# Optimization experiments

Measured on AMD Instinct MI355X. Metric: run time of the kernel, lower is better.

Reference implementation:

```python
import jax, jax.numpy as jnp
import numpy as np
from jax import lax

B, T, C = 64, 1024, 256


def setup_inputs() -> dict:
    key = jax.random.key(0)
    k1, k2 = jax.random.split(key)
    sequences = jax.random.normal(k1, (B, T, C), dtype=jnp.float32)
    transitions = jax.random.normal(k2, (C, C), dtype=jnp.float32)
    return {"sequences": sequences, "transitions": transitions}


def _viterbi_decode(sequences, transitions):
    # sequences: [B, T, C] unary scores; transitions: [C_prev, C_cur]
    num_classes = sequences.shape[-1]
    emissions = jnp.swapaxes(sequences, 0, 1)  # [T, B, C]

    def fwd_step(alpha, emit):
        # alpha: [B, C_prev]; emit: [B, C_cur]
        m = alpha[:, :, None] + transitions[None, :, :]  # [B, C_prev, C_cur]
        bp = jnp.argmax(m, axis=1).astype(jnp.int32)     # [B, C_cur] backpointers
        new_alpha = jnp.max(m, axis=1) + emit            # [B, C_cur]
        return new_alpha, bp

    alpha, bps = lax.scan(fwd_step, emissions[0], emissions[1:])  # bps: [T-1, B, C]
    last_tag = jnp.argmax(alpha, axis=-1).astype(jnp.int32)       # [B]

    def back_step(tag, bp):
        # tag: [B] tag at t+1; bp: [B, C] backpointers computed at step t+1
        prev = jnp.take_along_axis(bp, tag[:, None], axis=1)[:, 0]
        return prev, prev

    _, tags = lax.scan(back_step, last_tag, bps, reverse=True)  # [T-1, B]
    full = jnp.concatenate([tags, last_tag[None, :]], axis=0)   # [T, B]
    return jnp.swapaxes(full, 0, 1)  # [B, T]


def reference(sequences, transitions):
    # Inference path of CRF.call: viterbi decode + one-hot over num_classes.
    tags = _viterbi_decode(sequences, transitions)
    return jax.nn.one_hot(tags, sequences.shape[-1], dtype=sequences.dtype)
```

## Files before the change

### kernel.cpp

```cpp
#include <hip/hip_runtime.h>

#define Bn 64
#define Tn 1024
#define Cn 256

#define FWD_SYNC()                                  \
  do {                                              \
    __builtin_amdgcn_sched_barrier(0);              \
    __builtin_amdgcn_s_waitcnt(0xC07F);             \
    __builtin_amdgcn_s_barrier();                   \
    __builtin_amdgcn_sched_barrier(0);              \
  } while (0)

template<int CTRL>
__device__ __forceinline__ float dpp_mov_f(float x) {
  return __int_as_float(__builtin_amdgcn_update_dpp(0, __float_as_int(x), CTRL, 0xF, 0xF, true));
}
template<int CTRL>
__device__ __forceinline__ void max_stage(float& v) {
  const float pv = __int_as_float(__builtin_amdgcn_update_dpp(
      (int)0xFF800000, __float_as_int(v), CTRL, 0xF, 0xF, false));
  v = fmaxf(v, pv);
}

__device__ __forceinline__ int argmax64_fast(float v, int i) {
  float mv = v;
  max_stage<0x111>(mv);
  max_stage<0x112>(mv);
  max_stage<0x114>(mv);
  max_stage<0x118>(mv);
  max_stage<0x142>(mv);
  max_stage<0x143>(mv);
  const float smax = __int_as_float(__builtin_amdgcn_readlane(__float_as_int(mv), 63));
  const unsigned long long m = __ballot(v == smax);
  const int ln = __ffsll((unsigned long long)m) - 1;
  return __builtin_amdgcn_readlane(i, ln);
}

__device__ __forceinline__ int apad(int m) { return (m >> 2) * 20 + (m & 3) * 4; }

__global__ __launch_bounds__(1024) void crf_fwd_kernel(
    float* __restrict__ seq, const float* __restrict__ trans,
    float* __restrict__ transT, int useT) {
  __shared__ float lds[64 * 65];
  const int bi = blockIdx.x;
  const int tid = threadIdx.x;

  if (bi < Bn) {
    float* sb = seq + (size_t)bi * (Tn * Cn);
    const int l = tid & 63;
    const int w = tid >> 6;
    const int c = l & 15;
    const int g = l >> 4;
    const int ccb = w * 16 + g * 4;
    const int cpb = c * 16;
    float4 tr4[16];
#pragma unroll
    for (int k = 0; k < 16; ++k)
      tr4[k] = *(const float4*)(trans + (size_t)(cpb + k) * Cn + ccb);

    float* ab0 = lds;
    float* ab1 = lds + 320;
    if (tid < 64) *(float4*)(ab0 + apad(tid)) = ((const float4*)sb)[tid];
    const bool leader = (c == 0);
    const int woff = apad(w * 4 + g);
    float4 e4, pna;
    if (leader) e4 = *(const float4*)(sb + Cn + ccb);
    FWD_SYNC();

    for (int t = 1; t < Tn; ++t) {
      float4 pf;
      if (leader) {
        if (t > 1) *(float4*)(sb + (size_t)(t - 1) * Cn + ccb) = pna;
        const int tn = (t + 1 < Tn) ? (t + 1) : (Tn - 1);
        pf = *(const float4*)(sb + (size_t)tn * Cn + ccb);
      }
      const float* av = (t & 1) ? ab0 : ab1;
      float* aw = (t & 1) ? ab1 : ab0;
      const float* avc = av + c * 20;
      float m0 = -__builtin_inff(), m1 = m0, m2 = m0, m3 = m0;
#pragma unroll
      for (int j = 0; j < 4; ++j) {
        const float4 a = *(const float4*)(avc + j * 4);
        float4 t0 = tr4[4 * j + 0];
        m0 = fmaxf(m0, a.x + t0.x); m1 = fmaxf(m1, a.x + t0.y);
        m2 = fmaxf(m2, a.x + t0.z); m3 = fmaxf(m3, a.x + t0.w);
        float4 t1 = tr4[4 * j + 1];
        m0 = fmaxf(m0, a.y + t1.x); m1 = fmaxf(m1, a.y + t1.y);
        m2 = fmaxf(m2, a.y + t1.z); m3 = fmaxf(m3, a.y + t1.w);
        float4 t2 = tr4[4 * j + 2];
        m0 = fmaxf(m0, a.z + t2.x); m1 = fmaxf(m1, a.z + t2.y);
        m2 = fmaxf(m2, a.z + t2.z); m3 = fmaxf(m3, a.z + t2.w);
        float4 t3 = tr4[4 * j + 3];
        m0 = fmaxf(m0, a.w + t3.x); m1 = fmaxf(m1, a.w + t3.y);
        m2 = fmaxf(m2, a.w + t3.z); m3 = fmaxf(m3, a.w + t3.w);
      }
      m0 = fmaxf(m0, dpp_mov_f<0x128>(m0)); m1 = fmaxf(m1, dpp_mov_f<0x128>(m1));
      m2 = fmaxf(m2, dpp_mov_f<0x128>(m2)); m3 = fmaxf(m3, dpp_mov_f<0x128>(m3));
      m0 = fmaxf(m0, dpp_mov_f<0x124>(m0)); m1 = fmaxf(m1, dpp_mov_f<0x124>(m1));
      m2 = fmaxf(m2, dpp_mov_f<0x124>(m2)); m3 = fmaxf(m3, dpp_mov_f<0x124>(m3));
      m0 = fmaxf(m0, dpp_mov_f<0x122>(m0)); m1 = fmaxf(m1, dpp_mov_f<0x122>(m1));
      m2 = fmaxf(m2, dpp_mov_f<0x122>(m2)); m3 = fmaxf(m3, dpp_mov_f<0x122>(m3));
      m0 = fmaxf(m0, dpp_mov_f<0x121>(m0)); m1 = fmaxf(m1, dpp_mov_f<0x121>(m1));
      m2 = fmaxf(m2, dpp_mov_f<0x121>(m2)); m3 = fmaxf(m3, dpp_mov_f<0x121>(m3));
      if (leader) {
        float4 na;
        na.x = m0 + e4.x; na.y = m1 + e4.y; na.z = m2 + e4.z; na.w = m3 + e4.w;
        *(float4*)(aw + woff) = na;
        pna = na;
        e4 = pf;
      }
      FWD_SYNC();
    }
    if (leader) *(float4*)(sb + (size_t)(Tn - 1) * Cn + ccb) = pna;
  } else if (useT) {
    const int idx = bi - Bn;
    const int ti = idx >> 2, tj = idx & 3;
    const int tx = tid & 63, ty = tid >> 6;
#pragma unroll
    for (int q = 0; q < 4; ++q) {
      const int row = q * 16 + ty;
      lds[tx * 65 + row] = trans[(size_t)(ti * 64 + row) * Cn + tj * 64 + tx];
    }
    __syncthreads();
#pragma unroll
    for (int q = 0; q < 4; ++q) {
      const int row = q * 16 + ty;
      transT[(size_t)(tj * 64 + row) * Cn + ti * 64 + tx] = lds[row * 65 + tx];
    }
  }
}

__device__ __forceinline__ float4 onehot4(int tg, int cp0) {
  float4 z;
  z.x = (tg == cp0 + 0) ? 1.0f : 0.0f; z.y = (tg == cp0 + 1) ? 1.0f : 0.0f;
  z.z = (tg == cp0 + 2) ? 1.0f : 0.0f; z.w = (tg == cp0 + 3) ? 1.0f : 0.0f;
  return z;
}

template<int K>
__device__ __forceinline__ int chain_chunk(
    const float* __restrict__ A, int* __restrict__ tags,
    const float* __restrict__ transT, int tag, int l) {
  const int cp0 = l * 4;
#pragma unroll
  for (int k = 0; k < K; ++k) {
    const float4 tv = *(const float4*)(transT + (size_t)tag * Cn + cp0);
    const float4 ac = *(const float4*)(A + k * Cn + cp0);
    float v = ac.x + tv.x; int i = cp0;
    float vv; bool cnd;
    vv = ac.y + tv.y; cnd = vv > v; v = cnd ? vv : v; i = cnd ? cp0 + 1 : i;
    vv = ac.z + tv.z; cnd = vv > v; v = cnd ? vv : v; i = cnd ? cp0 + 2 : i;
    vv = ac.w + tv.w; cnd = vv > v; v = cnd ? vv : v; i = cnd ? cp0 + 3 : i;
    tag = argmax64_fast(v, i);
    if (l == 0) tags[k] = tag;
  }
  return tag;
}

__global__ __launch_bounds__(256) void crf_bwd_kernel(
    const float* __restrict__ seq, const float* __restrict__ trans,
    const float* __restrict__ transT, float* __restrict__ out, int useT) {
  __shared__ float aL[2][16][Cn];
  __shared__ int tagL[2][16];
  const int b = blockIdx.x;
  const int tid = threadIdx.x;
  const int wv = tid >> 6;
  const int l = tid & 63;
  const int cp0 = l * 4;
  const float* sb = seq + (size_t)b * (Tn * Cn);
  float* ob = out + (size_t)b * (Tn * Cn);

  if (!useT) {
    if (wv == 0) {
      float4 a = *(const float4*)(sb + (size_t)(Tn - 1) * Cn + cp0);
      float v = a.x; int i = cp0; bool cnd;
      cnd = a.y > v; v = cnd ? a.y : v; i = cnd ? cp0 + 1 : i;
      cnd = a.z > v; v = cnd ? a.z : v; i = cnd ? cp0 + 2 : i;
      cnd = a.w > v; v = cnd ? a.w : v; i = cnd ? cp0 + 3 : i;
      int tag = argmax64_fast(v, i);
      *(float4*)(ob + (size_t)(Tn - 1) * Cn + cp0) = onehot4(tag, cp0);
      for (int t = Tn - 2; t >= 0; --t) {
        const float4 ac = *(const float4*)(sb + (size_t)t * Cn + cp0);
        float4 tv;
        tv.x = trans[(size_t)(cp0 + 0) * Cn + tag];
        tv.y = trans[(size_t)(cp0 + 1) * Cn + tag];
        tv.z = trans[(size_t)(cp0 + 2) * Cn + tag];
        tv.w = trans[(size_t)(cp0 + 3) * Cn + tag];
        float v2 = ac.x + tv.x; int i2 = cp0; float vv; bool c2;
        vv = ac.y + tv.y; c2 = vv > v2; v2 = c2 ? vv : v2; i2 = c2 ? cp0 + 1 : i2;
        vv = ac.z + tv.z; c2 = vv > v2; v2 = c2 ? vv : v2; i2 = c2 ? cp0 + 2 : i2;
        vv = ac.w + tv.w; c2 = vv > v2; v2 = c2 ? vv : v2; i2 = c2 ? cp0 + 3 : i2;
        tag = argmax64_fast(v2, i2);
        *(float4*)(ob + (size_t)t * Cn + cp0) = onehot4(tag, cp0);
      }
    }
    return;
  }

  int tag = 0;
  if (wv == 0) {
    float4 a = *(const float4*)(sb + (size_t)(Tn - 1) * Cn + cp0);
    float v = a.x; int i = cp0; bool cnd;
    cnd = a.y > v; v = cnd ? a.y : v; i = cnd ? cp0 + 1 : i;
    cnd = a.z > v; v = cnd ? a.z : v; i = cnd ? cp0 + 2 : i;
    cnd = a.w > v; v = cnd ? a.w : v; i = cnd ? cp0 + 3 : i;
    tag = argmax64_fast(v, i);
    *(float4*)(ob + (size_t)(Tn - 1) * Cn + cp0) = onehot4(tag, cp0);
  } else if (wv <= 2) {
    const int s0 = (wv == 1) ? 0 : 8, s1 = (wv == 1) ? 8 : 15;
    for (int s = s0; s < s1; ++s)
      *(float4*)(&aL[0][s][cp0]) = *(const float4*)(sb + (size_t)(1022 - s) * Cn + cp0);
  }
  __syncthreads();

  int p = 0, t0 = 1022, K = 15, pt0 = 0, pK = 0;
  for (int ch = 0; ch < 64; ++ch) {
    const int nt0 = t0 - K;
    if (wv == 0) {
      if (ch == 0) tag = chain_chunk<15>(&aL[p][0][0], tagL[p], transT, tag, l);
      else        tag = chain_chunk<16>(&aL[p][0][0], tagL[p], transT, tag, l);
    } else if (wv <= 2) {
      if (ch < 63) {
        const int s0 = (wv == 1) ? 0 : 8, s1 = (wv == 1) ? 8 : 16;
        for (int s = s0; s < s1; ++s)
          *(float4*)(&aL[1 - p][s][cp0]) =
              *(const float4*)(sb + (size_t)(nt0 - s) * Cn + cp0);
      }
    } else {
      if (ch > 0) {
        for (int k = 0; k < pK; ++k)
          *(float4*)(ob + (size_t)(pt0 - k) * Cn + cp0) =
              onehot4(tagL[1 - p][k], cp0);
      }
    }
    __syncthreads();
    pt0 = t0; pK = K; t0 = nt0; K = 16; p ^= 1;
  }
  if (wv == 3) {
    for (int k = 0; k < 16; ++k)
      *(float4*)(ob + (size_t)(15 - k) * Cn + cp0) = onehot4(tagL[1][k], cp0);
  }
}

extern "C" void kernel_launch(void* const* d_in, const int* in_sizes, int n_in,
                              void* d_out, int out_size, void* d_ws, size_t ws_size,
                              hipStream_t stream) {
  float* seq = (float*)d_in[0];
  const float* trans = (const float*)d_in[1];
  float* out = (float*)d_out;
  float* transT = (float*)d_ws;
  const int useT = (ws_size >= (size_t)Cn * Cn * sizeof(float)) ? 1 : 0;

  crf_fwd_kernel<<<dim3(Bn + 16), dim3(1024), 0, stream>>>(seq, trans, transT, useT);
  crf_bwd_kernel<<<dim3(Bn), dim3(256), 0, stream>>>(seq, trans, transT, out, useT);
}
```

Before: 1.309 ms.

## Use plain syncthreads in forward loop and nontemporal loads/stores in backward pass

Replaces the custom sched_barrier/waitcnt/s_barrier macro in the forward recurrence with __syncthreads, adds a min-blocks hint to the forward kernel's launch bounds, and switches the backward pass's alpha reloads and one-hot output writes to nontemporal loads and stores. The nontemporal accesses are meant to avoid polluting caches with streamed data. The sync change may make the waits more conservative, stalling on outstanding global prefetches and stores every step of the serial loop. The launch-bounds hint may constrain register allocation.

```diff
diff --git a/kernel.cpp b/kernel.cpp
--- a/kernel.cpp
+++ b/kernel.cpp
@@ -4,13 +4,16 @@
 #define Tn 1024
 #define Cn 256
 
-#define FWD_SYNC()                                  \
-  do {                                              \
-    __builtin_amdgcn_sched_barrier(0);              \
-    __builtin_amdgcn_s_waitcnt(0xC07F);             \
-    __builtin_amdgcn_s_barrier();                   \
-    __builtin_amdgcn_sched_barrier(0);              \
-  } while (0)
+typedef float nv4 __attribute__((ext_vector_type(4)));
+
+__device__ __forceinline__ float4 nt_load4(const float* p) {
+  nv4 r = __builtin_nontemporal_load((const nv4*)p);
+  return make_float4(r.x, r.y, r.z, r.w);
+}
+__device__ __forceinline__ void nt_store4(float* p, float4 v) {
+  nv4 r = {v.x, v.y, v.z, v.w};
+  __builtin_nontemporal_store(r, (nv4*)p);
+}
 
 template<int CTRL>
 __device__ __forceinline__ float dpp_mov_f(float x) {
@@ -39,7 +42,7 @@
 
 __device__ __forceinline__ int apad(int m) { return (m >> 2) * 20 + (m & 3) * 4; }
 
-__global__ __launch_bounds__(1024) void crf_fwd_kernel(
+__global__ __launch_bounds__(1024, 4) void crf_fwd_kernel(
     float* __restrict__ seq, const float* __restrict__ trans,
     float* __restrict__ transT, int useT) {
   __shared__ float lds[64 * 65];
@@ -66,7 +69,7 @@
     const int woff = apad(w * 4 + g);
     float4 e4, pna;
     if (leader) e4 = *(const float4*)(sb + Cn + ccb);
-    FWD_SYNC();
+    __syncthreads();
 
     for (int t = 1; t < Tn; ++t) {
       float4 pf;
@@ -110,7 +113,7 @@
         pna = na;
         e4 = pf;
       }
-      FWD_SYNC();
+      __syncthreads();
     }
     if (leader) *(float4*)(sb + (size_t)(Tn - 1) * Cn + ccb) = pna;
   } else if (useT) {
@@ -210,7 +213,7 @@
   } else if (wv <= 2) {
     const int s0 = (wv == 1) ? 0 : 8, s1 = (wv == 1) ? 8 : 15;
     for (int s = s0; s < s1; ++s)
-      *(float4*)(&aL[0][s][cp0]) = *(const float4*)(sb + (size_t)(1022 - s) * Cn + cp0);
+      *(float4*)(&aL[0][s][cp0]) = nt_load4(sb + (size_t)(1022 - s) * Cn + cp0);
   }
   __syncthreads();
 
@@ -224,14 +227,12 @@
       if (ch < 63) {
         const int s0 = (wv == 1) ? 0 : 8, s1 = (wv == 1) ? 8 : 16;
         for (int s = s0; s < s1; ++s)
-          *(float4*)(&aL[1 - p][s][cp0]) =
-              *(const float4*)(sb + (size_t)(nt0 - s) * Cn + cp0);
+          *(float4*)(&aL[1 - p][s][cp0]) = nt_load4(sb + (size_t)(nt0 - s) * Cn + cp0);
       }
     } else {
       if (ch > 0) {
         for (int k = 0; k < pK; ++k)
-          *(float4*)(ob + (size_t)(pt0 - k) * Cn + cp0) =
-              onehot4(tagL[1 - p][k], cp0);
+          nt_store4(ob + (size_t)(pt0 - k) * Cn + cp0, onehot4(tagL[1 - p][k], cp0));
       }
     }
     __syncthreads();
@@ -239,7 +240,7 @@
   }
   if (wv == 3) {
     for (int k = 0; k < 16; ++k)
-      *(float4*)(ob + (size_t)(15 - k) * Cn + cp0) = onehot4(tagL[1][k], cp0);
+      nt_store4(ob + (size_t)(15 - k) * Cn + cp0, onehot4(tagL[1][k], cp0));
   }
 }
 
```

Result: faster. 1.266 ms (-3.3%).
